# Kernel tuning notes

Hardware: AMD Instinct MI355X
Metric: run time of the kernel (lower is better)

Reference implementation:

```python
import jax, jax.numpy as jnp
import numpy as np

N_NODES = 200000
N_EDGES = 600000
F_IN, F_HID, F_OUT = 165, 128, 2


def gcn_conv(x, edge_index, W, b):
    # PyG GCNConv: add self-loops, symmetric deg^{-1/2} normalization,
    # linear transform, scatter-add aggregation (src -> dst), then bias.
    N = x.shape[0]
    loop = jnp.arange(N, dtype=edge_index.dtype)
    src = jnp.concatenate([edge_index[0], loop])
    dst = jnp.concatenate([edge_index[1], loop])
    deg = jax.ops.segment_sum(jnp.ones_like(dst, dtype=x.dtype), dst, num_segments=N)
    dinv = jnp.where(deg > 0, jax.lax.rsqrt(jnp.maximum(deg, 1e-12)), 0.0)
    norm = dinv[src] * dinv[dst]              # [E+N]
    h = x @ W                                  # [N, out]
    msg = h[src] * norm[:, None]               # gather + scale
    out = jax.ops.segment_sum(msg, dst, num_segments=N)  # scatter-add
    return out + b


def setup_inputs() -> dict:
    key = jax.random.key(0)
    k1, k2, k3, k4, k5 = jax.random.split(key, 5)
    x = jax.random.normal(k1, (N_NODES, F_IN), dtype=jnp.float32)
    edge_index = jax.random.randint(k2, (2, N_EDGES), 0, N_NODES, dtype=jnp.int64)
    # Glorot-style init for GCN weights, zero bias (as in PyG GCNConv).
    W1 = jax.random.normal(k3, (F_IN, F_HID), dtype=jnp.float32) / np.sqrt(F_IN)
    b1 = jnp.zeros((F_HID,), dtype=jnp.float32)
    W2 = jax.random.normal(k4, (F_HID, F_OUT), dtype=jnp.float32) / np.sqrt(F_HID)
    b2 = jnp.zeros((F_OUT,), dtype=jnp.float32)
    return {"x": x, "edge_index": edge_index, "W1": W1, "b1": b1, "W2": W2, "b2": b2}


def reference(x, edge_index, W1, b1, W2, b2):
    h = gcn_conv(x, edge_index, W1, b1)
    h = jax.nn.relu(h)
    # dropout(p=0.5) is identity in eval mode
    out = gcn_conv(h, edge_index, W2, b2)
    return out
```

## Files before the change

### kernel.cpp

```cpp
#include <hip/hip_runtime.h>

#define N_NODES 200000
#define N_EDGES 600000
#define F_IN 165
#define F_HID 128
#define KP 200

typedef short short8 __attribute__((ext_vector_type(8)));
typedef float f32x4 __attribute__((ext_vector_type(4)));

__device__ __forceinline__ unsigned short f2bf(float f) {
  union { float f; unsigned int u; } v; v.f = f;
  unsigned int u = v.u;
  return (unsigned short)((u + 0x7FFFu + ((u >> 16) & 1u)) >> 16);
}
__device__ __forceinline__ float bflo(unsigned int v) {
  union { unsigned int u; float f; } x; x.u = v << 16; return x.f;
}
__device__ __forceinline__ float bfhi(unsigned int v) {
  union { unsigned int u; float f; } x; x.u = v & 0xffff0000u; return x.f;
}

__global__ void k_zero(int* __restrict__ cnt) {
  int i = blockIdx.x * 256 + threadIdx.x;
  if (i < N_NODES) cnt[i] = 0;
}

__global__ void k_count(const int* __restrict__ ei, int* __restrict__ cnt) {
  int e = blockIdx.x * 256 + threadIdx.x;
  if (e < N_EDGES) atomicAdd(&cnt[ei[N_EDGES + e]], 1);
}

__global__ void k_scan1(const int* __restrict__ cnt, int* __restrict__ rowptr, int* __restrict__ bsum) {
  __shared__ int sd[256];
  int t = threadIdx.x;
  int idx = blockIdx.x * 256 + t;
  int v = (idx < N_NODES) ? cnt[idx] : 0;
  sd[t] = v; __syncthreads();
  #pragma unroll
  for (int off = 1; off < 256; off <<= 1) {
    int u = (t >= off) ? sd[t - off] : 0;
    __syncthreads();
    sd[t] += u;
    __syncthreads();
  }
  if (idx < N_NODES) rowptr[idx] = sd[t] - v;
  if (t == 255) bsum[blockIdx.x] = sd[t];
}

__global__ void k_scan2(int* __restrict__ bsum, int nb) {
  __shared__ int sd[1024];
  int t = threadIdx.x;
  int v = (t < nb) ? bsum[t] : 0;
  sd[t] = v; __syncthreads();
  for (int off = 1; off < 1024; off <<= 1) {
    int u = (t >= off) ? sd[t - off] : 0;
    __syncthreads();
    sd[t] += u;
    __syncthreads();
  }
  if (t < nb) bsum[t] = sd[t] - v;
}

__global__ void k_scan3(const int* __restrict__ cnt, const int* __restrict__ bsum,
                        int* __restrict__ rowptr, int* __restrict__ fill, float* __restrict__ dinv) {
  int idx = blockIdx.x * 256 + threadIdx.x;
  if (idx < N_NODES) {
    int rp = rowptr[idx] + bsum[blockIdx.x];
    rowptr[idx] = rp;
    fill[idx] = rp;
    dinv[idx] = rsqrtf((float)(cnt[idx] + 1));
  }
  if (idx == 0) rowptr[N_NODES] = N_EDGES;
}

__global__ void k_fill(const int* __restrict__ ei, int* __restrict__ fill, int* __restrict__ srcl) {
  int e = blockIdx.x * 256 + threadIdx.x;
  if (e < N_EDGES) {
    int d = ei[N_EDGES + e];
    int s = ei[e];
    int slot = atomicAdd(&fill[d], 1);
    srcl[slot] = s;
  }
}

__global__ void k_wt(const float* __restrict__ W1, unsigned short* __restrict__ wt) {
  int idx = blockIdx.x * 256 + threadIdx.x;
  if (idx < F_HID * KP) {
    int c = idx / KP, k = idx - c * KP;
    wt[idx] = (k < F_IN) ? f2bf(W1[k * F_HID + c]) : (unsigned short)0;
  }
}

__global__ __launch_bounds__(256) void k_gemm1(const float* __restrict__ x,
                                               const unsigned short* __restrict__ wt,
                                               const float* __restrict__ dinv,
                                               unsigned short* __restrict__ h16) {
  __shared__ unsigned short As[32 * KP];
  __shared__ unsigned short Bs[F_HID * KP];
  int tid = threadIdx.x;

  const uint4* wt4 = (const uint4*)wt;
  uint4* Bs4 = (uint4*)Bs;
  #pragma unroll 4
  for (int j = tid; j < F_HID * KP / 8; j += 256) Bs4[j] = wt4[j];

  long r0 = (long)blockIdx.x * 32;
  const float4* x4 = (const float4*)(x + r0 * F_IN);
  for (int j = tid; j < 32 * F_IN / 4; j += 256) {
    float4 v = x4[j];
    int e = 4 * j;
    #pragma unroll
    for (int u = 0; u < 4; ++u) {
      int ee = e + u;
      int r = ee / F_IN, c = ee - r * F_IN;
      As[r * KP + c] = f2bf((&v.x)[u]);
    }
  }
  for (int j = tid; j < 32 * (KP - F_IN); j += 256) {
    int r = j / (KP - F_IN), c = F_IN + (j - r * (KP - F_IN));
    As[r * KP + c] = 0;
  }
  __syncthreads();

  int lane = tid & 63;
  int w = tid >> 6;
  int rg = w & 1;
  int ch = w >> 1;
  int arow = rg * 16 + (lane & 15);
  int kg = (lane >> 4) * 8;
  f32x4 acc[4];
  #pragma unroll
  for (int i = 0; i < 4; ++i) acc[i] = (f32x4){0.f, 0.f, 0.f, 0.f};
  #pragma unroll
  for (int ks = 0; ks < 6; ++ks) {
    short8 af = *(const short8*)(&As[arow * KP + ks * 32 + kg]);
    #pragma unroll
    for (int cb = 0; cb < 4; ++cb) {
      int col = (ch * 4 + cb) * 16 + (lane & 15);
      short8 bf = *(const short8*)(&Bs[col * KP + ks * 32 + kg]);
      acc[cb] = __builtin_amdgcn_mfma_f32_16x16x32_bf16(af, bf, acc[cb], 0, 0, 0);
    }
  }
  long orow = r0 + rg * 16 + (lane >> 4) * 4;
  int ocol = lane & 15;
  float dv[4];
  #pragma unroll
  for (int j = 0; j < 4; ++j) dv[j] = dinv[orow + j];
  #pragma unroll
  for (int cb = 0; cb < 4; ++cb) {
    #pragma unroll
    for (int j = 0; j < 4; ++j) {
      h16[(orow + j) * F_HID + (ch * 4 + cb) * 16 + ocol] = f2bf(acc[cb][j] * dv[j]);
    }
  }
}

__global__ __launch_bounds__(256) void k_agg1(const unsigned int* __restrict__ H,
                                              const float* __restrict__ dinv,
                                              const int* __restrict__ rowptr, const int* __restrict__ srcl,
                                              const float* __restrict__ b1, const float* __restrict__ W2,
                                              float* __restrict__ h2s) {
  int tid = threadIdx.x;
  int local = tid >> 6;
  int lane = tid & 63;
  int d = blockIdx.x * 4 + local;

  unsigned int v = H[(long)d * 64 + lane];
  float acc0 = bflo(v), acc1 = bfhi(v);
  int r0 = rowptr[d], r1 = rowptr[d + 1];
  int n = r1 - r0;
  for (int b = 0; b < n; b += 4) {
    int i0 = r0 + b;
    bool m1 = b + 1 < n, m2 = b + 2 < n, m3 = b + 3 < n;
    int s0 = srcl[i0];
    int s1 = m1 ? srcl[i0 + 1] : s0;
    int s2 = m2 ? srcl[i0 + 2] : s0;
    int s3 = m3 ? srcl[i0 + 3] : s0;
    unsigned int v0 = H[(long)s0 * 64 + lane];
    unsigned int v1 = H[(long)s1 * 64 + lane];
    unsigned int v2 = H[(long)s2 * 64 + lane];
    unsigned int v3 = H[(long)s3 * 64 + lane];
    acc0 += bflo(v0);                      acc1 += bfhi(v0);
    acc0 = fmaf(m1 ? 1.f : 0.f, bflo(v1), acc0); acc1 = fmaf(m1 ? 1.f : 0.f, bfhi(v1), acc1);
    acc0 = fmaf(m2 ? 1.f : 0.f, bflo(v2), acc0); acc1 = fmaf(m2 ? 1.f : 0.f, bfhi(v2), acc1);
    acc0 = fmaf(m3 ? 1.f : 0.f, bflo(v3), acc0); acc1 = fmaf(m3 ? 1.f : 0.f, bfhi(v3), acc1);
  }
  float dd = dinv[d];
  float2 bb = ((const float2*)b1)[lane];
  float a0 = fmaxf(fmaf(acc0, dd, bb.x), 0.f);
  float a1 = fmaxf(fmaf(acc1, dd, bb.y), 0.f);
  float4 w2 = ((const float4*)W2)[lane];
  float p0 = a0 * w2.x + a1 * w2.z;
  float p1 = a0 * w2.y + a1 * w2.w;
  #pragma unroll
  for (int off = 32; off > 0; off >>= 1) {
    p0 += __shfl_down(p0, off);
    p1 += __shfl_down(p1, off);
  }
  if (lane == 0) ((float2*)h2s)[d] = make_float2(p0 * dd, p1 * dd);
}

__global__ void k_agg2(const float* __restrict__ h2s, const float* __restrict__ dinv,
                       const int* __restrict__ rowptr, const int* __restrict__ srcl,
                       const float* __restrict__ b2, float* __restrict__ out) {
  int d = blockIdx.x * 256 + threadIdx.x;
  if (d >= N_NODES) return;
  const float2* G = (const float2*)h2s;
  float2 g = G[d];
  float o0 = g.x, o1 = g.y;
  int r0 = rowptr[d], r1 = rowptr[d + 1];
  int n = r1 - r0;
  for (int b = 0; b < n; b += 4) {
    int i0 = r0 + b;
    bool m1 = b + 1 < n, m2 = b + 2 < n, m3 = b + 3 < n;
    int s0 = srcl[i0];
    int s1 = m1 ? srcl[i0 + 1] : s0;
    int s2 = m2 ? srcl[i0 + 2] : s0;
    int s3 = m3 ? srcl[i0 + 3] : s0;
    float2 g0 = G[s0], g1 = G[s1], g2 = G[s2], g3 = G[s3];
    o0 += g0.x;                   o1 += g0.y;
    o0 = fmaf(m1 ? 1.f : 0.f, g1.x, o0); o1 = fmaf(m1 ? 1.f : 0.f, g1.y, o1);
    o0 = fmaf(m2 ? 1.f : 0.f, g2.x, o0); o1 = fmaf(m2 ? 1.f : 0.f, g2.y, o1);
    o0 = fmaf(m3 ? 1.f : 0.f, g3.x, o0); o1 = fmaf(m3 ? 1.f : 0.f, g3.y, o1);
  }
  float dd = dinv[d];
  ((float2*)out)[d] = make_float2(fmaf(o0, dd, b2[0]), fmaf(o1, dd, b2[1]));
}

extern "C" void kernel_launch(void* const* d_in, const int* in_sizes, int n_in,
                              void* d_out, int out_size, void* d_ws, size_t ws_size,
                              hipStream_t stream) {
  const float* x  = (const float*)d_in[0];
  const int*   ei = (const int*)d_in[1];
  const float* W1 = (const float*)d_in[2];
  const float* b1 = (const float*)d_in[3];
  const float* W2 = (const float*)d_in[4];
  const float* b2 = (const float*)d_in[5];
  float* out = (float*)d_out;

  char* p = (char*)d_ws;
  size_t off = 0;
  auto take = [&](size_t bytes) -> void* {
    void* r = p + off;
    off += (bytes + 255) & ~(size_t)255;
    return r;
  };
  unsigned short* h16    = (unsigned short*)take((size_t)N_NODES * F_HID * 2);
  unsigned short* wt     = (unsigned short*)take((size_t)F_HID * KP * 2);
  float*          h2s    = (float*)take((size_t)N_NODES * 2 * 4);
  int*            cnt    = (int*)take((size_t)N_NODES * 4);
  int*            fill   = (int*)take((size_t)N_NODES * 4);
  int*            rowptr = (int*)take(((size_t)N_NODES + 1) * 4);
  int*            srcl   = (int*)take(((size_t)N_EDGES + 8) * 4);
  float*          dinv   = (float*)take((size_t)N_NODES * 4);
  int*            bsum   = (int*)take(4096);
  (void)ws_size; (void)in_sizes; (void)n_in; (void)out_size;

  int nbE = (N_EDGES + 255) / 256;
  int nbN = (N_NODES + 255) / 256;
  k_zero<<<nbN, 256, 0, stream>>>(cnt);
  k_count<<<nbE, 256, 0, stream>>>(ei, cnt);
  k_scan1<<<nbN, 256, 0, stream>>>(cnt, rowptr, bsum);
  k_scan2<<<1, 1024, 0, stream>>>(bsum, nbN);
  k_scan3<<<nbN, 256, 0, stream>>>(cnt, bsum, rowptr, fill, dinv);
  k_fill<<<nbE, 256, 0, stream>>>(ei, fill, srcl);
  k_wt<<<(F_HID * KP + 255) / 256, 256, 0, stream>>>(W1, wt);
  k_gemm1<<<N_NODES / 32, 256, 0, stream>>>(x, wt, dinv, h16);
  k_agg1<<<N_NODES / 4, 256, 0, stream>>>((const unsigned int*)h16, dinv, rowptr, srcl, b1, W2, h2s);
  k_agg2<<<nbN, 256, 0, stream>>>(h2s, dinv, rowptr, srcl, b2, out);
}
```

Baseline: 213.0 us.

## Make gemm1 persistent with register-prefetched next x tile

The first-layer GEMM becomes a persistent kernel: 512 blocks loop over the 6250 row tiles, so the 51KB weight tile is loaded into shared memory once per block instead of once per 32-row tile. While the MFMAs run on the current tile, each thread prefetches the next x tile into registers and writes it to shared memory after a barrier. This adds register pressure and two barriers per tile, and may reduce occupancy or latency hiding compared with the many-block launch.

Result: faster. 185.0 us (-13.1%).

```diff
diff --git a/kernel.cpp b/kernel.cpp
--- a/kernel.cpp
+++ b/kernel.cpp
@@ -5,6 +5,7 @@
 #define F_IN 165
 #define F_HID 128
 #define KP 200
+#define NT 6250
 
 typedef short short8 __attribute__((ext_vector_type(8)));
 typedef float f32x4 __attribute__((ext_vector_type(4)));
@@ -96,8 +97,8 @@
                                                const unsigned short* __restrict__ wt,
                                                const float* __restrict__ dinv,
                                                unsigned short* __restrict__ h16) {
+  __shared__ unsigned short Bs[F_HID * KP];
   __shared__ unsigned short As[32 * KP];
-  __shared__ unsigned short Bs[F_HID * KP];
   int tid = threadIdx.x;
 
   const uint4* wt4 = (const uint4*)wt;
@@ -105,21 +106,26 @@
   #pragma unroll 4
   for (int j = tid; j < F_HID * KP / 8; j += 256) Bs4[j] = wt4[j];
 
-  long r0 = (long)blockIdx.x * 32;
-  const float4* x4 = (const float4*)(x + r0 * F_IN);
-  for (int j = tid; j < 32 * F_IN / 4; j += 256) {
-    float4 v = x4[j];
-    int e = 4 * j;
-    #pragma unroll
-    for (int u = 0; u < 4; ++u) {
-      int ee = e + u;
-      int r = ee / F_IN, c = ee - r * F_IN;
-      As[r * KP + c] = f2bf((&v.x)[u]);
-    }
-  }
   for (int j = tid; j < 32 * (KP - F_IN); j += 256) {
-    int r = j / (KP - F_IN), c = F_IN + (j - r * (KP - F_IN));
+    int r = j / (KP - F_IN), c = F_IN + (j - (j / (KP - F_IN)) * (KP - F_IN));
     As[r * KP + c] = 0;
+  }
+
+  int t = blockIdx.x;
+  int G = gridDim.x;
+
+  {
+    const float4* x4 = (const float4*)(x + (long)t * 32 * F_IN);
+    for (int j = tid; j < 32 * F_IN / 4; j += 256) {
+      float4 v = x4[j];
+      int e = 4 * j;
+      #pragma unroll
+      for (int u = 0; u < 4; ++u) {
+        int ee = e + u;
+        int r = ee / F_IN, c = ee - r * F_IN;
+        As[r * KP + c] = f2bf((&v.x)[u]);
+      }
+    }
   }
   __syncthreads();
 
@@ -129,30 +135,65 @@
   int ch = w >> 1;
   int arow = rg * 16 + (lane & 15);
   int kg = (lane >> 4) * 8;
-  f32x4 acc[4];
-  #pragma unroll
-  for (int i = 0; i < 4; ++i) acc[i] = (f32x4){0.f, 0.f, 0.f, 0.f};
-  #pragma unroll
-  for (int ks = 0; ks < 6; ++ks) {
-    short8 af = *(const short8*)(&As[arow * KP + ks * 32 + kg]);
+
+  while (t < NT) {
+    int tn = t + G;
+    bool have = tn < NT;
+
+    float4 vals[6];
+    if (have) {
+      const float4* x4 = (const float4*)(x + (long)tn * 32 * F_IN);
+      #pragma unroll
+      for (int i = 0; i < 6; ++i) {
+        int j = tid + i * 256;
+        if (j < 32 * F_IN / 4) vals[i] = x4[j];
+      }
+    }
+
+    f32x4 acc[4];
+    #pragma unroll
+    for (int i = 0; i < 4; ++i) acc[i] = (f32x4){0.f, 0.f, 0.f, 0.f};
+    #pragma unroll
+    for (int ks = 0; ks < 6; ++ks) {
+      short8 af = *(const short8*)(&As[arow * KP + ks * 32 + kg]);
+      #pragma unroll
+      for (int cb = 0; cb < 4; ++cb) {
+        int col = (ch * 4 + cb) * 16 + (lane & 15);
+        short8 bf = *(const short8*)(&Bs[col * KP + ks * 32 + kg]);
+        acc[cb] = __builtin_amdgcn_mfma_f32_16x16x32_bf16(af, bf, acc[cb], 0, 0, 0);
+      }
+    }
+    long orow = (long)t * 32 + rg * 16 + (lane >> 4) * 4;
+    int ocol = lane & 15;
+    float dv[4];
+    #pragma unroll
+    for (int j = 0; j < 4; ++j) dv[j] = dinv[orow + j];
     #pragma unroll
     for (int cb = 0; cb < 4; ++cb) {
-      int col = (ch * 4 + cb) * 16 + (lane & 15);
-      short8 bf = *(const short8*)(&Bs[col * KP + ks * 32 + kg]);
-      acc[cb] = __builtin_amdgcn_mfma_f32_16x16x32_bf16(af, bf, acc[cb], 0, 0, 0);
-    }
-  }
-  long orow = r0 + rg * 16 + (lane >> 4) * 4;
-  int ocol = lane & 15;
-  float dv[4];
-  #pragma unroll
-  for (int j = 0; j < 4; ++j) dv[j] = dinv[orow + j];
-  #pragma unroll
-  for (int cb = 0; cb < 4; ++cb) {
-    #pragma unroll
-    for (int j = 0; j < 4; ++j) {
-      h16[(orow + j) * F_HID + (ch * 4 + cb) * 16 + ocol] = f2bf(acc[cb][j] * dv[j]);
-    }
+      #pragma unroll
+      for (int j = 0; j < 4; ++j) {
+        h16[(orow + j) * F_HID + (ch * 4 + cb) * 16 + ocol] = f2bf(acc[cb][j] * dv[j]);
+      }
+    }
+    __syncthreads();
+
+    if (have) {
+      #pragma unroll
+      for (int i = 0; i < 6; ++i) {
+        int j = tid + i * 256;
+        if (j < 32 * F_IN / 4) {
+          int e = 4 * j;
+          #pragma unroll
+          for (int u = 0; u < 4; ++u) {
+            int ee = e + u;
+            int r = ee / F_IN, c = ee - r * F_IN;
+            As[r * KP + c] = f2bf((&vals[i].x)[u]);
+          }
+        }
+      }
+    }
+    __syncthreads();
+    t = tn;
   }
 }
 
@@ -266,7 +307,7 @@
   k_scan3<<<nbN, 256, 0, stream>>>(cnt, bsum, rowptr, fill, dinv);
   k_fill<<<nbE, 256, 0, stream>>>(ei, fill, srcl);
   k_wt<<<(F_HID * KP + 255) / 256, 256, 0, stream>>>(W1, wt);
-  k_gemm1<<<N_NODES / 32, 256, 0, stream>>>(x, wt, dinv, h16);
+  k_gemm1<<<512, 256, 0, stream>>>(x, wt, dinv, h16);
   k_agg1<<<N_NODES / 4, 256, 0, stream>>>((const unsigned int*)h16, dinv, rowptr, srcl, b1, W2, h2s);
   k_agg2<<<nbN, 256, 0, stream>>>(h2s, dinv, rowptr, srcl, b2, out);
 }
```

## Make GEMM1 persistent with register-resident weights and direct x loads

Applied to the files above, without the earlier changes.

Rewrites the first GEMM as a persistent kernel. Each wave keeps its half of the bf16-transposed weight matrix in registers and loops over 16-row tiles, loading x straight from global memory into MFMA fragments instead of staging A and B through shared memory. It also folds the weight-transpose kernel into the zero kernel to drop a launch. This removes the per-block 51KB shared-memory reload of W and the LDS staging, at the cost of heavy register use (48 short8 fragments) and uncoalesced strided scalar x loads.

New measurement: 191.8 us. -10.0%, faster.

```diff
diff --git a/kernel.cpp b/kernel.cpp
--- a/kernel.cpp
+++ b/kernel.cpp
@@ -5,6 +5,7 @@
 #define F_IN 165
 #define F_HID 128
 #define KP 200
+#define NRT 12500
 
 typedef short short8 __attribute__((ext_vector_type(8)));
 typedef float f32x4 __attribute__((ext_vector_type(4)));
@@ -21,9 +22,14 @@
   union { unsigned int u; float f; } x; x.u = v & 0xffff0000u; return x.f;
 }
 
-__global__ void k_zero(int* __restrict__ cnt) {
+__global__ void k_zero(int* __restrict__ cnt, const float* __restrict__ W1,
+                       unsigned short* __restrict__ wt) {
   int i = blockIdx.x * 256 + threadIdx.x;
   if (i < N_NODES) cnt[i] = 0;
+  if (i < F_HID * KP) {
+    int c = i / KP, k = i - c * KP;
+    wt[i] = (k < F_IN) ? f2bf(W1[k * F_HID + c]) : (unsigned short)0;
+  }
 }
 
 __global__ void k_count(const int* __restrict__ ei, int* __restrict__ cnt) {
@@ -84,74 +90,67 @@
   }
 }
 
-__global__ void k_wt(const float* __restrict__ W1, unsigned short* __restrict__ wt) {
-  int idx = blockIdx.x * 256 + threadIdx.x;
-  if (idx < F_HID * KP) {
-    int c = idx / KP, k = idx - c * KP;
-    wt[idx] = (k < F_IN) ? f2bf(W1[k * F_HID + c]) : (unsigned short)0;
-  }
-}
-
 __global__ __launch_bounds__(256) void k_gemm1(const float* __restrict__ x,
                                                const unsigned short* __restrict__ wt,
                                                const float* __restrict__ dinv,
                                                unsigned short* __restrict__ h16) {
-  __shared__ unsigned short As[32 * KP];
-  __shared__ unsigned short Bs[F_HID * KP];
   int tid = threadIdx.x;
-
-  const uint4* wt4 = (const uint4*)wt;
-  uint4* Bs4 = (uint4*)Bs;
-  #pragma unroll 4
-  for (int j = tid; j < F_HID * KP / 8; j += 256) Bs4[j] = wt4[j];
-
-  long r0 = (long)blockIdx.x * 32;
-  const float4* x4 = (const float4*)(x + r0 * F_IN);
-  for (int j = tid; j < 32 * F_IN / 4; j += 256) {
-    float4 v = x4[j];
-    int e = 4 * j;
-    #pragma unroll
-    for (int u = 0; u < 4; ++u) {
-      int ee = e + u;
-      int r = ee / F_IN, c = ee - r * F_IN;
-      As[r * KP + c] = f2bf((&v.x)[u]);
-    }
-  }
-  for (int j = tid; j < 32 * (KP - F_IN); j += 256) {
-    int r = j / (KP - F_IN), c = F_IN + (j - r * (KP - F_IN));
-    As[r * KP + c] = 0;
-  }
-  __syncthreads();
-
   int lane = tid & 63;
-  int w = tid >> 6;
-  int rg = w & 1;
-  int ch = w >> 1;
-  int arow = rg * 16 + (lane & 15);
-  int kg = (lane >> 4) * 8;
-  f32x4 acc[4];
-  #pragma unroll
-  for (int i = 0; i < 4; ++i) acc[i] = (f32x4){0.f, 0.f, 0.f, 0.f};
-  #pragma unroll
-  for (int ks = 0; ks < 6; ++ks) {
-    short8 af = *(const short8*)(&As[arow * KP + ks * 32 + kg]);
+  int gw = blockIdx.x * 4 + (tid >> 6);
+  int nw = gridDim.x * 4;
+  int cw = gw & 1;
+  int lane15 = lane & 15;
+  int kq = (lane >> 4) * 8;
+
+  short8 wf[4][6];
+  {
+    int c0 = cw * 64 + lane15;
     #pragma unroll
     for (int cb = 0; cb < 4; ++cb) {
-      int col = (ch * 4 + cb) * 16 + (lane & 15);
-      short8 bf = *(const short8*)(&Bs[col * KP + ks * 32 + kg]);
-      acc[cb] = __builtin_amdgcn_mfma_f32_16x16x32_bf16(af, bf, acc[cb], 0, 0, 0);
-    }
-  }
-  long orow = r0 + rg * 16 + (lane >> 4) * 4;
-  int ocol = lane & 15;
-  float dv[4];
-  #pragma unroll
-  for (int j = 0; j < 4; ++j) dv[j] = dinv[orow + j];
-  #pragma unroll
-  for (int cb = 0; cb < 4; ++cb) {
-    #pragma unroll
-    for (int j = 0; j < 4; ++j) {
-      h16[(orow + j) * F_HID + (ch * 4 + cb) * 16 + ocol] = f2bf(acc[cb][j] * dv[j]);
+      #pragma unroll
+      for (int ks = 0; ks < 6; ++ks) {
+        wf[cb][ks] = *(const short8*)(&wt[(c0 + cb * 16) * KP + ks * 32 + kq]);
+      }
+    }
+  }
+
+  for (int t = gw >> 1; t < NRT; t += (nw >> 1)) {
+    long r = (long)t * 16 + lane15;
+    const float* xr = x + r * F_IN;
+
+    short8 xf[6];
+    #pragma unroll
+    for (int ks = 0; ks < 6; ++ks) {
+      int k0 = ks * 32 + kq;
+      short8 s;
+      #pragma unroll
+      for (int j = 0; j < 8; ++j) {
+        float vv = (ks * 32 + 31 < F_IN) ? xr[k0 + j]
+                 : ((k0 + j < F_IN) ? xr[k0 + j] : 0.f);
+        s[j] = (short)f2bf(vv);
+      }
+      xf[ks] = s;
+    }
+
+    f32x4 acc[4];
+    #pragma unroll
+    for (int i = 0; i < 4; ++i) acc[i] = (f32x4){0.f, 0.f, 0.f, 0.f};
+    #pragma unroll
+    for (int ks = 0; ks < 6; ++ks) {
+      #pragma unroll
+      for (int cb = 0; cb < 4; ++cb) {
+        acc[cb] = __builtin_amdgcn_mfma_f32_16x16x32_bf16(wf[cb][ks], xf[ks], acc[cb], 0, 0, 0);
+      }
+    }
+
+    float dd = dinv[r];
+    unsigned short* hp = &h16[r * F_HID + cw * 64 + (lane >> 4) * 4];
+    #pragma unroll
+    for (int cb = 0; cb < 4; ++cb) {
+      unsigned int p0 = (unsigned int)f2bf(acc[cb][0] * dd) | ((unsigned int)f2bf(acc[cb][1] * dd) << 16);
+      unsigned int p1 = (unsigned int)f2bf(acc[cb][2] * dd) | ((unsigned int)f2bf(acc[cb][3] * dd) << 16);
+      uint2 pp; pp.x = p0; pp.y = p1;
+      *(uint2*)(hp + cb * 16) = pp;
     }
   }
 }
@@ -259,14 +258,13 @@
 
   int nbE = (N_EDGES + 255) / 256;
   int nbN = (N_NODES + 255) / 256;
-  k_zero<<<nbN, 256, 0, stream>>>(cnt);
+  k_zero<<<nbN, 256, 0, stream>>>(cnt, W1, wt);
   k_count<<<nbE, 256, 0, stream>>>(ei, cnt);
   k_scan1<<<nbN, 256, 0, stream>>>(cnt, rowptr, bsum);
   k_scan2<<<1, 1024, 0, stream>>>(bsum, nbN);
   k_scan3<<<nbN, 256, 0, stream>>>(cnt, bsum, rowptr, fill, dinv);
   k_fill<<<nbE, 256, 0, stream>>>(ei, fill, srcl);
-  k_wt<<<(F_HID * KP + 255) / 256, 256, 0, stream>>>(W1, wt);
-  k_gemm1<<<N_NODES / 32, 256, 0, stream>>>(x, wt, dinv, h16);
+  k_gemm1<<<1024, 256, 0, stream>>>(x, wt, dinv, h16);
   k_agg1<<<N_NODES / 4, 256, 0, stream>>>((const unsigned int*)h16, dinv, rowptr, srcl, b1, W2, h2s);
   k_agg2<<<nbN, 256, 0, stream>>>(h2s, dinv, rowptr, srcl, b2, out);
 }
```
